# Kernel optimization log

Measured on AMD Instinct MI355X. Metric: run time of the kernel, lower is better.

Reference implementation:

```python
import jax, jax.numpy as jnp
import numpy as np

NUM_USERS = 200000
NUM_ARTISTS = 50000
LATENT_DIM = 64
NUM_EDGES = 2000000
NUM_LAYERS = 3


def setup_inputs() -> dict:
    key = jax.random.key(0)
    k_u, k_a, k_src, k_dst = jax.random.split(key, 4)
    x_users = jax.random.normal(k_u, (NUM_USERS, LATENT_DIM), dtype=jnp.float32)
    x_artists = jax.random.normal(k_a, (NUM_ARTISTS, LATENT_DIM), dtype=jnp.float32)
    # a2u: row 0 = artist (source) ids, row 1 = user (target) ids
    art = jax.random.randint(k_src, (NUM_EDGES,), 0, NUM_ARTISTS, dtype=jnp.int32)
    usr = jax.random.randint(k_dst, (NUM_EDGES,), 0, NUM_USERS, dtype=jnp.int32)
    edge_index_a2u = jnp.stack([art, usr], axis=0)
    # u2a is the reversed edge list: row 0 = user (source), row 1 = artist (target)
    edge_index_u2a = jnp.stack([usr, art], axis=0)
    return {
        "x_users": x_users,
        "x_artists": x_artists,
        "edge_index_a2u": edge_index_a2u,
        "edge_index_u2a": edge_index_u2a,
    }


def _scatter_mean(src_nodes, edge_index, dim_size):
    """Gather src_nodes[edge_index[0]] and scatter-mean onto edge_index[1].

    Matches torch_scatter.scatter(reduce='mean'): empty segments yield 0.
    """
    msgs = src_nodes[edge_index[0]]                     # [E, D] gather
    sums = jax.ops.segment_sum(msgs, edge_index[1], num_segments=dim_size)
    ones = jnp.ones((edge_index.shape[1],), dtype=src_nodes.dtype)
    counts = jax.ops.segment_sum(ones, edge_index[1], num_segments=dim_size)
    return sums / jnp.maximum(counts, 1.0)[:, None]


def reference(x_users, x_artists, edge_index_a2u, edge_index_u2a):
    scale = 1.0 / (NUM_LAYERS + 1)
    final_u = x_users * scale
    final_a = x_artists * scale
    for _ in range(NUM_LAYERS):
        x_users = _scatter_mean(x_artists, edge_index_a2u, NUM_USERS)
        x_artists = _scatter_mean(x_users, edge_index_u2a, NUM_ARTISTS)
        final_u = final_u + x_users * scale
        final_a = final_a + x_artists * scale
    return final_u, final_a
```

## Files before the change

kernel.cpp:

```cpp
#include <hip/hip_runtime.h>
#include <hip/hip_fp16.h>

#define D 64
#define TB 256

#define BSHIFT_U 10
#define BSHIFT_A 8
#define SHARDS 8
#define SCAP   1536
#define CAP    (SHARDS * SCAP)
#define CAPC_U 16384
#define CAPC_A 12288
#define TSHIFT 14
#define PCHUNK 2048

typedef _Float16 half8 __attribute__((ext_vector_type(8)));
typedef float float8 __attribute__((ext_vector_type(8)));
typedef float f32x4 __attribute__((ext_vector_type(4)));

__device__ __forceinline__ float8 h8_to_f8(half8 h) {
    return __builtin_convertvector(h, float8);
}
template <typename T>
__device__ __forceinline__ T ntl(const T* p) { return __builtin_nontemporal_load(p); }
template <typename T>
__device__ __forceinline__ void nts(T* p, T v) { __builtin_nontemporal_store(v, p); }

__global__ __launch_bounds__(TB) void cvt_f16_kernel(const f32x4* __restrict__ in,
                                                     half8* __restrict__ out, int n8) {
    int i = blockIdx.x * blockDim.x + threadIdx.x;
    int stride = gridDim.x * blockDim.x;
    for (int j = i; j < n8; j += stride) {
        f32x4 a = in[j * 2 + 0];
        f32x4 b = in[j * 2 + 1];
        half8 h;
        h[0] = (_Float16)a[0]; h[1] = (_Float16)a[1]; h[2] = (_Float16)a[2]; h[3] = (_Float16)a[3];
        h[4] = (_Float16)b[0]; h[5] = (_Float16)b[1]; h[6] = (_Float16)b[2]; h[7] = (_Float16)b[3];
        out[j] = h;
    }
}

struct PartShared {
    unsigned sorted[PCHUNK];
    unsigned short loc[PCHUNK];
    int cnt[256];
    int gbase[256];
    int seg[256];
    int scanbuf[TB];
};

__global__ __launch_bounds__(TB) void partition_both_kernel(const int* __restrict__ art,
                                                            const int* __restrict__ usr, int E,
                                                            int* __restrict__ bcur_u,
                                                            int* __restrict__ bcur_a,
                                                            unsigned* __restrict__ part_u,
                                                            unsigned* __restrict__ part_a,
                                                            int NBu, int NBa) {
    __shared__ PartShared sh;
    const int tid = threadIdx.x;
    const int dir = blockIdx.x & 1;
    const int cidx = blockIdx.x >> 1;
    const int shard = cidx & (SHARDS - 1);
    const int c0 = cidx * PCHUNK;
    if (c0 >= E) return;
    const int m = min(PCHUNK, E - c0);
    const int NB = dir ? NBa : NBu;
    const int BSH = dir ? BSHIFT_A : BSHIFT_U;
    const int* key = dir ? art : usr;
    int* bcur = dir ? bcur_a : bcur_u;
    unsigned* part = dir ? part_a : part_u;

    for (int i = tid; i < NB; i += TB) sh.cnt[i] = 0;
    __syncthreads();
    for (int i = tid; i < m; i += TB) {
        int b = key[c0 + i] >> BSH;
        sh.loc[i] = (unsigned short)atomicAdd(&sh.cnt[b], 1);
    }
    __syncthreads();
    int v = (tid < NB) ? sh.cnt[tid] : 0;
    sh.scanbuf[tid] = v;
    __syncthreads();
    for (int off = 1; off < TB; off <<= 1) {
        int t = (tid >= off) ? sh.scanbuf[tid - off] : 0;
        __syncthreads();
        if (tid >= off) sh.scanbuf[tid] += t;
        __syncthreads();
    }
    if (tid < NB) {
        sh.seg[tid] = sh.scanbuf[tid] - v;
        if (v) {
            int old = atomicAdd(&bcur[tid * SHARDS + shard], v);
            sh.gbase[tid] = tid * CAP + shard * SCAP + old;
        }
    }
    __syncthreads();
    const unsigned mask = (1u << BSH) - 1u;
    for (int i = tid; i < m; i += TB) {
        int a = art[c0 + i], u = usr[c0 + i];
        int k = dir ? a : u;
        int s = dir ? u : a;
        int b = k >> BSH;
        sh.sorted[sh.seg[b] + sh.loc[i]] = ((unsigned)s << BSH) | ((unsigned)k & mask);
    }
    __syncthreads();
    const int wid = tid >> 6;
    const int lane = tid & 63;
    for (int b = wid; b < NB; b += TB / 64) {
        int s = sh.seg[b];
        int send = (b + 1 < NB) ? sh.seg[b + 1] : m;
        if (send <= s) continue;
        unsigned* dst = part + (size_t)sh.gbase[b];
        for (int i = s + lane; i < send; i += 64) dst[i - s] = sh.sorted[i];
    }
}

template <int NPB, int NB, int BSHIFT>
__device__ __forceinline__ void local_csr_body(const unsigned* __restrict__ part,
                                               const int* __restrict__ shard_cnt,
                                               int ebeg_p, int ebeg_c, int n0,
                                               int2* __restrict__ rowdeg,
                                               int* __restrict__ csr, int N,
                                               int* cnt, int* sdata) {
    const int tid = threadIdx.x;
    const int NBINS = NPB * NB;
    const unsigned mask = (unsigned)(NPB - 1);
    int cs[SHARDS];
    for (int s = 0; s < SHARDS; ++s) cs[s] = shard_cnt[s];
    for (int i = tid; i < NBINS; i += TB) cnt[i] = 0;
    __syncthreads();
    for (int s = 0; s < SHARDS; ++s) {
        const int base = ebeg_p + s * SCAP;
        const int endv = base + cs[s];
        for (int e = base + tid; e < endv; e += TB) {
            unsigned r = part[e];
            int bin = (int)(r & mask) * NB + (int)((r >> BSHIFT) >> TSHIFT);
            atomicAdd(&cnt[bin], 1);
        }
    }
    __syncthreads();
    const int ITEMS = NBINS / TB;
    const int NPT = ITEMS / NB;
    const int ib = tid * ITEMS;
    int dj[NPT], pdj[NPT], nsj[NPT];
    int local = 0;
    for (int j = 0; j < NPT; ++j) {
        int d = 0;
        for (int k = 0; k < NB; ++k) d += cnt[ib + j * NB + k];
        dj[j] = d;
        pdj[j] = (d + 3) & ~3;
        local += pdj[j];
    }
    sdata[tid] = local;
    __syncthreads();
    for (int off = 1; off < TB; off <<= 1) {
        int t = (tid >= off) ? sdata[tid - off] : 0;
        __syncthreads();
        if (tid >= off) sdata[tid] += t;
        __syncthreads();
    }
    int run = sdata[tid] - local;
    for (int j = 0; j < NPT; ++j) {
        nsj[j] = run;
        int c = run;
        for (int k = 0; k < NB; ++k) {
            int idx = ib + j * NB + k;
            int v = cnt[idx];
            cnt[idx] = c;
            c += v;
        }
        int n = n0 + tid * NPT + j;
        if (n < N) rowdeg[n] = make_int2(ebeg_c + run, dj[j]);
        run += pdj[j];
    }
    __syncthreads();
    for (int s = 0; s < SHARDS; ++s) {
        const int base = ebeg_p + s * SCAP;
        const int endv = base + cs[s];
        for (int e = base + tid; e < endv; e += TB) {
            unsigned r = part[e];
            int bin = (int)(r & mask) * NB + (int)((r >> BSHIFT) >> TSHIFT);
            int pos = atomicAdd(&cnt[bin], 1);
            csr[ebeg_c + pos] = (int)(r >> BSHIFT);
        }
    }
    for (int j = 0; j < NPT; ++j)
        for (int k = dj[j]; k < pdj[j]; ++k) csr[ebeg_c + nsj[j] + k] = 0;
}

__global__ __launch_bounds__(TB) void local_csr_both_kernel(const unsigned* __restrict__ part_u,
                                                            const unsigned* __restrict__ part_a,
                                                            const int* __restrict__ bcur_u,
                                                            const int* __restrict__ bcur_a,
                                                            int2* __restrict__ rowdeg_u,
                                                            int2* __restrict__ rowdeg_a,
                                                            int* __restrict__ csr_u,
                                                            int* __restrict__ csr_a,
                                                            int NU, int NA, int NBu) {
    __shared__ int cnt[4096];
    __shared__ int sdata[TB];
    const int b = blockIdx.x;
    if (b < NBu) {
        local_csr_body<1024, 4, BSHIFT_U>(part_u, bcur_u + b * SHARDS, b * CAP, b * CAPC_U,
                                          b << BSHIFT_U, rowdeg_u, csr_u, NU, cnt, sdata);
    } else {
        const int bb = b - NBu;
        local_csr_body<256, 16, BSHIFT_A>(part_a, bcur_a + bb * SHARDS, bb * CAP, bb * CAPC_A,
                                          bb << BSHIFT_A, rowdeg_a, csr_a, NA, cnt, sdata);
    }
}

__global__ __launch_bounds__(TB) void gather_mean_kernel(const half8* __restrict__ src,
                                                         const int* __restrict__ csr,
                                                         const int2* __restrict__ rowdeg,
                                                         half8* __restrict__ x_out,
                                                         f32x4* __restrict__ final_acc,
                                                         const f32x4* __restrict__ init_src,
                                                         const f32x4* __restrict__ fin_in0,
                                                         const half8* __restrict__ fin_x1,
                                                         const half8* __restrict__ fin_x2,
                                                         f32x4* __restrict__ fin_out,
                                                         int N, float scale) {
    const int lane = threadIdx.x & 7;
    int g = (blockIdx.x * blockDim.x + threadIdx.x) >> 3;
    const int ngroups = (gridDim.x * blockDim.x) >> 3;
    const float8 r0 = h8_to_f8(src[lane]);
    for (int n = g; n < N; n += ngroups) {
        const int2 rd = rowdeg[n];
        const int beg = rd.x;
        const int dg = rd.y;
        const int pd = (dg + 3) & ~3;
        const int end = beg + pd;
        float8 a0 = 0.f, a1 = 0.f, a2 = 0.f, a3 = 0.f;
        int e = beg;
        for (; e + 8 <= end; e += 8) {
            const int s0 = csr[e + 0];
            const int s1 = csr[e + 1];
            const int s2 = csr[e + 2];
            const int s3 = csr[e + 3];
            const int s4 = csr[e + 4];
            const int s5 = csr[e + 5];
            const int s6 = csr[e + 6];
            const int s7 = csr[e + 7];
            const half8 v0 = src[s0 * 8 + lane];
            const half8 v1 = src[s1 * 8 + lane];
            const half8 v2 = src[s2 * 8 + lane];
            const half8 v3 = src[s3 * 8 + lane];
            const half8 v4 = src[s4 * 8 + lane];
            const half8 v5 = src[s5 * 8 + lane];
            const half8 v6 = src[s6 * 8 + lane];
            const half8 v7 = src[s7 * 8 + lane];
            a0 += h8_to_f8(v0);
            a1 += h8_to_f8(v1);
            a2 += h8_to_f8(v2);
            a3 += h8_to_f8(v3);
            a0 += h8_to_f8(v4);
            a1 += h8_to_f8(v5);
            a2 += h8_to_f8(v6);
            a3 += h8_to_f8(v7);
        }
        if (e < end) {
            const int s0 = csr[e + 0];
            const int s1 = csr[e + 1];
            const int s2 = csr[e + 2];
            const int s3 = csr[e + 3];
            a0 += h8_to_f8(src[s0 * 8 + lane]);
            a1 += h8_to_f8(src[s1 * 8 + lane]);
            a2 += h8_to_f8(src[s2 * 8 + lane]);
            a3 += h8_to_f8(src[s3 * 8 + lane]);
        }
        float8 s = (a0 + a1) + (a2 + a3);
        s -= (float)(pd - dg) * r0;
        const float inv = 1.f / (float)(dg > 0 ? dg : 1);
        float8 x = s * inv;
        const int o8 = n * 8 + lane;
        if (x_out != nullptr) {
            half8 h;
            for (int k = 0; k < 8; ++k) h[k] = (_Float16)x[k];
            x_out[o8] = h;
        }
        const int fo = n * (D / 4) + lane * 2;
        if (fin_out != nullptr) {
            float8 t = h8_to_f8(ntl(&fin_x1[o8])) + h8_to_f8(ntl(&fin_x2[o8])) + x;
            f32x4 f0 = ntl(&fin_in0[fo + 0]);
            f32x4 f1 = ntl(&fin_in0[fo + 1]);
            f32x4 t0 = {t[0], t[1], t[2], t[3]};
            f32x4 t1 = {t[4], t[5], t[6], t[7]};
            nts(&fin_out[fo + 0], (f0 + t0) * scale);
            nts(&fin_out[fo + 1], (f1 + t1) * scale);
        }
        if (final_acc != nullptr) {
            f32x4 f0, f1;
            if (init_src != nullptr) {
                f0 = init_src[fo + 0] * scale;
                f1 = init_src[fo + 1] * scale;
            } else {
                f0 = final_acc[fo + 0];
                f1 = final_acc[fo + 1];
            }
            f32x4 x0 = {x[0], x[1], x[2], x[3]};
            f32x4 x1 = {x[4], x[5], x[6], x[7]};
            final_acc[fo + 0] = f0 + x0 * scale;
            final_acc[fo + 1] = f1 + x1 * scale;
        }
    }
}

extern "C" void kernel_launch(void* const* d_in, const int* in_sizes, int n_in,
                              void* d_out, int out_size, void* d_ws, size_t ws_size,
                              hipStream_t stream) {
    const float* x_users   = (const float*)d_in[0];
    const float* x_artists = (const float*)d_in[1];
    const int*   a2u       = (const int*)d_in[2];

    const int NU = in_sizes[0] / D;
    const int NA = in_sizes[1] / D;
    const int E  = in_sizes[2] / 2;
    const int* art = a2u;
    const int* usr = a2u + E;

    const float scale = 0.25f;

    const int NBu = (NU + (1 << BSHIFT_U) - 1) >> BSHIFT_U;
    const int NBa = (NA + (1 << BSHIFT_A) - 1) >> BSHIFT_A;

    char* w = (char*)d_ws;
    size_t off = 0;
    auto alloc = [&](size_t bytes) -> char* {
        char* p = w + off;
        off += (bytes + 255) & ~(size_t)255;
        return p;
    };
    int2* rowdeg_u = (int2*)alloc((size_t)NU * 8);
    int2* rowdeg_a = (int2*)alloc((size_t)NA * 8);
    int* bcur      = (int*)alloc((size_t)(NBu + NBa) * SHARDS * 4);
    int* bcur_u    = bcur;
    int* bcur_a    = bcur + NBu * SHARDS;
    int* csr_u     = (int*)alloc((size_t)NBu * CAPC_U * 4);
    int* csr_a     = (int*)alloc((size_t)NBa * CAPC_A * 4);
    half8* xa_in   = (half8*)alloc((size_t)NA * D * 2);
    unsigned* part_u = (unsigned*)alloc((size_t)NBu * CAP * 4);
    unsigned* part_a = (unsigned*)alloc((size_t)NBa * CAP * 4);

    const size_t XU = (size_t)NU * D * 2;
    const size_t XA = (size_t)NA * D * 2;
    const size_t XUa = (XU + 255) & ~(size_t)255;
    const size_t XAa = (XA + 255) & ~(size_t)255;

    const bool modeA = (off + 3 * XUa) <= ws_size;

    half8* x_u1 = (half8*)alloc(XU);
    half8* x_u2 = modeA ? (half8*)alloc(XU) : x_u1;
    half8* x_u3 = modeA ? (half8*)alloc(XU) : x_u1;
    char* part_base = (char*)part_u;
    half8* x_a1 = (half8*)(part_base);
    half8* x_a2 = modeA ? (half8*)(part_base + XAa) : x_a1;

    float* out_u = (float*)d_out;
    float* out_a = out_u + (size_t)NU * D;

    hipMemsetAsync(bcur, 0, (size_t)(NBu + NBa) * SHARDS * 4, stream);
    cvt_f16_kernel<<<1024, TB, 0, stream>>>((const f32x4*)x_artists, xa_in, NA * D / 8);
    const int nchunks = (E + PCHUNK - 1) / PCHUNK;
    partition_both_kernel<<<2 * nchunks, TB, 0, stream>>>(art, usr, E, bcur_u, bcur_a,
                                                          part_u, part_a, NBu, NBa);
    local_csr_both_kernel<<<NBu + NBa, TB, 0, stream>>>(part_u, part_a, bcur_u, bcur_a,
                                                        rowdeg_u, rowdeg_a,
                                                        csr_u, csr_a, NU, NA, NBu);

    half8* xu_buf[3] = {x_u1, x_u2, x_u3};
    half8* xa_buf[2] = {x_a1, x_a2};
    const half8* srcA = xa_in;
    for (int l = 0; l < 3; ++l) {
        const bool last = (l == 2);
        gather_mean_kernel<<<4096, TB, 0, stream>>>(
            srcA, csr_u, rowdeg_u, xu_buf[l],
            modeA ? nullptr : (f32x4*)out_u,
            (!modeA && l == 0) ? (const f32x4*)x_users : nullptr,
            (modeA && last) ? (const f32x4*)x_users : nullptr,
            (modeA && last) ? x_u1 : nullptr,
            (modeA && last) ? x_u2 : nullptr,
            (modeA && last) ? (f32x4*)out_u : nullptr,
            NU, scale);
        gather_mean_kernel<<<2048, TB, 0, stream>>>(
            xu_buf[l], csr_a, rowdeg_a,
            (modeA && last) ? nullptr : (modeA ? xa_buf[l] : x_a1),
            modeA ? nullptr : (f32x4*)out_a,
            (!modeA && l == 0) ? (const f32x4*)x_artists : nullptr,
            (modeA && last) ? (const f32x4*)x_artists : nullptr,
            (modeA && last) ? x_a1 : nullptr,
            (modeA && last) ? x_a2 : nullptr,
            (modeA && last) ? (f32x4*)out_a : nullptr,
            NA, scale);
        srcA = modeA ? xa_buf[l < 2 ? l : 0] : x_a1;
    }
}
```

Baseline: 350.8 us.

## Fold f16 conversion into partition kernel, use 16-bit user CSR, split gather lanes

Removes the separate f32-to-f16 conversion launch by running it on extra blocks appended to the partition kernel. Stores the artist-index CSR for the user-side gather as 16-bit values (artist ids are below 65536), halving index traffic. Templates the gather kernel on lanes per node, so the user-side gather uses 4-lane groups that each cover half of a row's columns. This changes how memory accesses are grouped and adds redundant index loads per split group, in exchange for more parallel groups per node.

```diff
diff --git a/kernel.cpp b/kernel.cpp
--- a/kernel.cpp
+++ b/kernel.cpp
@@ -26,20 +26,6 @@
 template <typename T>
 __device__ __forceinline__ void nts(T* p, T v) { __builtin_nontemporal_store(v, p); }
 
-__global__ __launch_bounds__(TB) void cvt_f16_kernel(const f32x4* __restrict__ in,
-                                                     half8* __restrict__ out, int n8) {
-    int i = blockIdx.x * blockDim.x + threadIdx.x;
-    int stride = gridDim.x * blockDim.x;
-    for (int j = i; j < n8; j += stride) {
-        f32x4 a = in[j * 2 + 0];
-        f32x4 b = in[j * 2 + 1];
-        half8 h;
-        h[0] = (_Float16)a[0]; h[1] = (_Float16)a[1]; h[2] = (_Float16)a[2]; h[3] = (_Float16)a[3];
-        h[4] = (_Float16)b[0]; h[5] = (_Float16)b[1]; h[6] = (_Float16)b[2]; h[7] = (_Float16)b[3];
-        out[j] = h;
-    }
-}
-
 struct PartShared {
     unsigned sorted[PCHUNK];
     unsigned short loc[PCHUNK];
@@ -49,15 +35,31 @@
     int scanbuf[TB];
 };
 
-__global__ __launch_bounds__(TB) void partition_both_kernel(const int* __restrict__ art,
-                                                            const int* __restrict__ usr, int E,
-                                                            int* __restrict__ bcur_u,
-                                                            int* __restrict__ bcur_a,
-                                                            unsigned* __restrict__ part_u,
-                                                            unsigned* __restrict__ part_a,
-                                                            int NBu, int NBa) {
+__global__ __launch_bounds__(TB) void partition_cvt_kernel(const int* __restrict__ art,
+                                                           const int* __restrict__ usr, int E,
+                                                           int* __restrict__ bcur_u,
+                                                           int* __restrict__ bcur_a,
+                                                           unsigned* __restrict__ part_u,
+                                                           unsigned* __restrict__ part_a,
+                                                           int NBu, int NBa,
+                                                           const f32x4* __restrict__ cvt_in,
+                                                           half8* __restrict__ cvt_out,
+                                                           int n8, int nPartBlocks) {
     __shared__ PartShared sh;
     const int tid = threadIdx.x;
+    if ((int)blockIdx.x >= nPartBlocks) {
+        int i = (blockIdx.x - nPartBlocks) * TB + tid;
+        int stride = (gridDim.x - nPartBlocks) * TB;
+        for (; i < n8; i += stride) {
+            f32x4 a = cvt_in[i * 2 + 0];
+            f32x4 b = cvt_in[i * 2 + 1];
+            half8 h;
+            h[0] = (_Float16)a[0]; h[1] = (_Float16)a[1]; h[2] = (_Float16)a[2]; h[3] = (_Float16)a[3];
+            h[4] = (_Float16)b[0]; h[5] = (_Float16)b[1]; h[6] = (_Float16)b[2]; h[7] = (_Float16)b[3];
+            cvt_out[i] = h;
+        }
+        return;
+    }
     const int dir = blockIdx.x & 1;
     const int cidx = blockIdx.x >> 1;
     const int shard = cidx & (SHARDS - 1);
@@ -114,12 +116,12 @@
     }
 }
 
-template <int NPB, int NB, int BSHIFT>
+template <int NPB, int NB, int BSHIFT, typename IT>
 __device__ __forceinline__ void local_csr_body(const unsigned* __restrict__ part,
                                                const int* __restrict__ shard_cnt,
                                                int ebeg_p, int ebeg_c, int n0,
                                                int2* __restrict__ rowdeg,
-                                               int* __restrict__ csr, int N,
+                                               IT* __restrict__ csr, int N,
                                                int* cnt, int* sdata) {
     const int tid = threadIdx.x;
     const int NBINS = NPB * NB;
@@ -180,11 +182,11 @@
             unsigned r = part[e];
             int bin = (int)(r & mask) * NB + (int)((r >> BSHIFT) >> TSHIFT);
             int pos = atomicAdd(&cnt[bin], 1);
-            csr[ebeg_c + pos] = (int)(r >> BSHIFT);
+            csr[ebeg_c + pos] = (IT)(r >> BSHIFT);
         }
     }
     for (int j = 0; j < NPT; ++j)
-        for (int k = dj[j]; k < pdj[j]; ++k) csr[ebeg_c + nsj[j] + k] = 0;
+        for (int k = dj[j]; k < pdj[j]; ++k) csr[ebeg_c + nsj[j] + k] = (IT)0;
 }
 
 __global__ __launch_bounds__(TB) void local_csr_both_kernel(const unsigned* __restrict__ part_u,
@@ -193,7 +195,7 @@
                                                             const int* __restrict__ bcur_a,
                                                             int2* __restrict__ rowdeg_u,
                                                             int2* __restrict__ rowdeg_a,
-                                                            int* __restrict__ csr_u,
+                                                            unsigned short* __restrict__ csr_u,
                                                             int* __restrict__ csr_a,
                                                             int NU, int NA, int NBu) {
     __shared__ int cnt[4096];
@@ -209,8 +211,9 @@
     }
 }
 
+template <int L, typename IT>
 __global__ __launch_bounds__(TB) void gather_mean_kernel(const half8* __restrict__ src,
-                                                         const int* __restrict__ csr,
+                                                         const IT* __restrict__ csr,
                                                          const int2* __restrict__ rowdeg,
                                                          half8* __restrict__ x_out,
                                                          f32x4* __restrict__ final_acc,
@@ -220,11 +223,16 @@
                                                          const half8* __restrict__ fin_x2,
                                                          f32x4* __restrict__ fin_out,
                                                          int N, float scale) {
-    const int lane = threadIdx.x & 7;
-    int g = (blockIdx.x * blockDim.x + threadIdx.x) >> 3;
-    const int ngroups = (gridDim.x * blockDim.x) >> 3;
-    const float8 r0 = h8_to_f8(src[lane]);
-    for (int n = g; n < N; n += ngroups) {
+    constexpr int SPLIT = 8 / L;
+    const int lane = threadIdx.x & (L - 1);
+    const int g = (blockIdx.x * blockDim.x + threadIdx.x) / L;
+    const int ngroups = (gridDim.x * blockDim.x) / L;
+    const int sub = g % SPLIT;
+    const int cb = sub * L + lane;
+    const int n0 = g / SPLIT;
+    const int nstride = ngroups / SPLIT;
+    const float8 r0 = h8_to_f8(src[cb]);
+    for (int n = n0; n < N; n += nstride) {
         const int2 rd = rowdeg[n];
         const int beg = rd.x;
         const int dg = rd.y;
@@ -233,22 +241,22 @@
         float8 a0 = 0.f, a1 = 0.f, a2 = 0.f, a3 = 0.f;
         int e = beg;
         for (; e + 8 <= end; e += 8) {
-            const int s0 = csr[e + 0];
-            const int s1 = csr[e + 1];
-            const int s2 = csr[e + 2];
-            const int s3 = csr[e + 3];
-            const int s4 = csr[e + 4];
-            const int s5 = csr[e + 5];
-            const int s6 = csr[e + 6];
-            const int s7 = csr[e + 7];
-            const half8 v0 = src[s0 * 8 + lane];
-            const half8 v1 = src[s1 * 8 + lane];
-            const half8 v2 = src[s2 * 8 + lane];
-            const half8 v3 = src[s3 * 8 + lane];
-            const half8 v4 = src[s4 * 8 + lane];
-            const half8 v5 = src[s5 * 8 + lane];
-            const half8 v6 = src[s6 * 8 + lane];
-            const half8 v7 = src[s7 * 8 + lane];
+            const int s0 = (int)csr[e + 0];
+            const int s1 = (int)csr[e + 1];
+            const int s2 = (int)csr[e + 2];
+            const int s3 = (int)csr[e + 3];
+            const int s4 = (int)csr[e + 4];
+            const int s5 = (int)csr[e + 5];
+            const int s6 = (int)csr[e + 6];
+            const int s7 = (int)csr[e + 7];
+            const half8 v0 = src[s0 * 8 + cb];
+            const half8 v1 = src[s1 * 8 + cb];
+            const half8 v2 = src[s2 * 8 + cb];
+            const half8 v3 = src[s3 * 8 + cb];
+            const half8 v4 = src[s4 * 8 + cb];
+            const half8 v5 = src[s5 * 8 + cb];
+            const half8 v6 = src[s6 * 8 + cb];
+            const half8 v7 = src[s7 * 8 + cb];
             a0 += h8_to_f8(v0);
             a1 += h8_to_f8(v1);
             a2 += h8_to_f8(v2);
@@ -259,26 +267,26 @@
             a3 += h8_to_f8(v7);
         }
         if (e < end) {
-            const int s0 = csr[e + 0];
-            const int s1 = csr[e + 1];
-            const int s2 = csr[e + 2];
-            const int s3 = csr[e + 3];
-            a0 += h8_to_f8(src[s0 * 8 + lane]);
-            a1 += h8_to_f8(src[s1 * 8 + lane]);
-            a2 += h8_to_f8(src[s2 * 8 + lane]);
-            a3 += h8_to_f8(src[s3 * 8 + lane]);
+            const int s0 = (int)csr[e + 0];
+            const int s1 = (int)csr[e + 1];
+            const int s2 = (int)csr[e + 2];
+            const int s3 = (int)csr[e + 3];
+            a0 += h8_to_f8(src[s0 * 8 + cb]);
+            a1 += h8_to_f8(src[s1 * 8 + cb]);
+            a2 += h8_to_f8(src[s2 * 8 + cb]);
+            a3 += h8_to_f8(src[s3 * 8 + cb]);
         }
         float8 s = (a0 + a1) + (a2 + a3);
         s -= (float)(pd - dg) * r0;
         const float inv = 1.f / (float)(dg > 0 ? dg : 1);
         float8 x = s * inv;
-        const int o8 = n * 8 + lane;
+        const int o8 = n * 8 + cb;
         if (x_out != nullptr) {
             half8 h;
             for (int k = 0; k < 8; ++k) h[k] = (_Float16)x[k];
             x_out[o8] = h;
         }
-        const int fo = n * (D / 4) + lane * 2;
+        const int fo = n * (D / 4) + cb * 2;
         if (fin_out != nullptr) {
             float8 t = h8_to_f8(ntl(&fin_x1[o8])) + h8_to_f8(ntl(&fin_x2[o8])) + x;
             f32x4 f0 = ntl(&fin_in0[fo + 0]);
@@ -335,7 +343,7 @@
     int* bcur      = (int*)alloc((size_t)(NBu + NBa) * SHARDS * 4);
     int* bcur_u    = bcur;
     int* bcur_a    = bcur + NBu * SHARDS;
-    int* csr_u     = (int*)alloc((size_t)NBu * CAPC_U * 4);
+    unsigned short* csr_u = (unsigned short*)alloc((size_t)NBu * CAPC_U * 2);
     int* csr_a     = (int*)alloc((size_t)NBa * CAPC_A * 4);
     half8* xa_in   = (half8*)alloc((size_t)NA * D * 2);
     unsigned* part_u = (unsigned*)alloc((size_t)NBu * CAP * 4);
@@ -359,10 +367,12 @@
     float* out_a = out_u + (size_t)NU * D;
 
     hipMemsetAsync(bcur, 0, (size_t)(NBu + NBa) * SHARDS * 4, stream);
-    cvt_f16_kernel<<<1024, TB, 0, stream>>>((const f32x4*)x_artists, xa_in, NA * D / 8);
     const int nchunks = (E + PCHUNK - 1) / PCHUNK;
-    partition_both_kernel<<<2 * nchunks, TB, 0, stream>>>(art, usr, E, bcur_u, bcur_a,
-                                                          part_u, part_a, NBu, NBa);
+    const int nPart = 2 * nchunks;
+    partition_cvt_kernel<<<nPart + 128, TB, 0, stream>>>(art, usr, E, bcur_u, bcur_a,
+                                                         part_u, part_a, NBu, NBa,
+                                                         (const f32x4*)x_artists, xa_in,
+                                                         NA * D / 8, nPart);
     local_csr_both_kernel<<<NBu + NBa, TB, 0, stream>>>(part_u, part_a, bcur_u, bcur_a,
                                                         rowdeg_u, rowdeg_a,
                                                         csr_u, csr_a, NU, NA, NBu);
@@ -372,7 +382,7 @@
     const half8* srcA = xa_in;
     for (int l = 0; l < 3; ++l) {
         const bool last = (l == 2);
-        gather_mean_kernel<<<4096, TB, 0, stream>>>(
+        gather_mean_kernel<4, unsigned short><<<4096, TB, 0, stream>>>(
             srcA, csr_u, rowdeg_u, xu_buf[l],
             modeA ? nullptr : (f32x4*)out_u,
             (!modeA && l == 0) ? (const f32x4*)x_users : nullptr,
@@ -381,7 +391,7 @@
             (modeA && last) ? x_u2 : nullptr,
             (modeA && last) ? (f32x4*)out_u : nullptr,
             NU, scale);
-        gather_mean_kernel<<<2048, TB, 0, stream>>>(
+        gather_mean_kernel<8, int><<<2048, TB, 0, stream>>>(
             xu_buf[l], csr_a, rowdeg_a,
             (modeA && last) ? nullptr : (modeA ? xa_buf[l] : x_a1),
             modeA ? nullptr : (f32x4*)out_a,
```

Result: faster. 333.1 us, median of 2 (-5.1%).
